# Performance work log

Hardware: AMD Instinct MI355X
Metric: run time of the kernel (lower is better)

The kernel has to match this reference:

```python
import jax, jax.numpy as jnp
import numpy as np

N_EMB = 1024
HEAD_SIZE = 128

def setup_inputs() -> dict:
    key = jax.random.key(0)
    kx, kq, kk, kv = jax.random.split(key, 4)
    s = 1.0 / np.sqrt(N_EMB)
    return {
        "x": jax.random.normal(kx, (4, 4096, N_EMB), dtype=jnp.float32),
        "Wq": jax.random.normal(kq, (N_EMB, HEAD_SIZE), dtype=jnp.float32) * s,
        "Wk": jax.random.normal(kk, (N_EMB, HEAD_SIZE), dtype=jnp.float32) * s,
        "Wv": jax.random.normal(kv, (N_EMB, HEAD_SIZE), dtype=jnp.float32) * s,
    }

def reference(x, Wq, Wk, Wv) -> jnp.ndarray:
    B, T, C = x.shape
    q = jnp.einsum('btc,cd->btd', x, Wq)  # [B,T,H]
    k = jnp.einsum('btc,cd->btd', x, Wk)
    v = jnp.einsum('btc,cd->btd', x, Wv)
    # NOTE: original scales by sqrt(n_emb), not sqrt(head_size)
    wei = jnp.einsum('btd,bsd->bts', q, k) / jnp.sqrt(jnp.asarray(C, x.dtype))
    causal = jnp.tril(jnp.ones((T, T), dtype=bool))
    wei = jnp.where(causal, wei, -jnp.inf)
    wei = jax.nn.softmax(wei, axis=-1)
    return jnp.einsum('bts,bsd->btd', wei, v)
```

## Files before the change

kernel.cpp:

```cpp
#include <hip/hip_runtime.h>
#include <hip/hip_bf16.h>


#define TSEQ 4096
#define NBATCH 4
#define CEMB 1024
#define HS 128
#define NWORK 272

typedef float  f32x4  __attribute__((ext_vector_type(4)));
typedef float  f32x16 __attribute__((ext_vector_type(16)));
typedef __bf16 bf16x4 __attribute__((ext_vector_type(4)));
typedef __bf16 bf16x8 __attribute__((ext_vector_type(8)));
typedef int    i32x2  __attribute__((ext_vector_type(2)));
typedef int    i32x4  __attribute__((ext_vector_type(4)));

__device__ __forceinline__ __bf16 f2b(float f) { return (__bf16)f; }
__device__ __forceinline__ float fexp2(float f) { return __builtin_amdgcn_exp2f(f); }

__device__ __forceinline__ void gl_lds16(const void* g, void* l) {
  __builtin_amdgcn_global_load_lds(
      (__attribute__((address_space(1))) void*)(g),
      (__attribute__((address_space(3))) void*)(l), 16, 0, 0);
}

__global__ void wtrans_kernel(const float* __restrict__ Wq,
                              const float* __restrict__ Wk,
                              const float* __restrict__ Wv,
                              __bf16* __restrict__ Wt) {
  const float* W = (blockIdx.y == 0) ? Wq : (blockIdx.y == 1) ? Wk : Wv;
  int g  = blockIdx.x * 256 + threadIdx.x;
  int n  = g & 127;
  int k0 = (g >> 7) * 8;
  bf16x8 v;
#pragma unroll
  for (int i = 0; i < 8; ++i) v[i] = f2b(W[(size_t)(k0 + i) * HS + n]);
  *(bf16x8*)(Wt + (size_t)blockIdx.y * HS * CEMB + (size_t)n * CEMB + k0) = v;
}

__global__ __launch_bounds__(128)
void proj_kernel(const float* __restrict__ x, const __bf16* __restrict__ Wt,
                 __bf16* __restrict__ qb, __bf16* __restrict__ kb,
                 __bf16* __restrict__ vt) {
  __shared__ __align__(16) __bf16 As[64 * 72];
  __shared__ __align__(16) __bf16 Bs[128 * 72];

  const int tid  = threadIdx.x;
  const int lane = tid & 63;
  const int w    = tid >> 6;
  const int l31  = lane & 31;
  const int half = lane >> 5;

  const int bid   = blockIdx.x;
  const int xcd   = bid & 7;
  const int rest  = bid >> 3;
  const int mat   = rest % 3;
  const int mslab = rest / 3;
  const int m0    = (xcd + 8 * mslab) * 64;
  const __bf16* Wm = Wt + (size_t)mat * HS * CEMB;

  f32x16 acc[2][2];
#pragma unroll
  for (int a = 0; a < 2; ++a)
#pragma unroll
    for (int b = 0; b < 2; ++b)
#pragma unroll
      for (int r = 0; r < 16; ++r) acc[a][b][r] = 0.f;

  const int srow = tid >> 3;
  const int soff = tid & 7;

  f32x4  pa[4][2];
  bf16x8 pb[8];
#pragma unroll
  for (int i = 0; i < 4; ++i) {
    const float* p = x + (size_t)(m0 + srow + 16 * i) * CEMB + soff * 8;
    pa[i][0] = *(const f32x4*)p;
    pa[i][1] = *(const f32x4*)(p + 4);
  }
#pragma unroll
  for (int i = 0; i < 8; ++i)
    pb[i] = *(const bf16x8*)(Wm + (size_t)(srow + 16 * i) * CEMB + soff * 8);

  for (int ks = 0; ks < CEMB; ks += 64) {
    __syncthreads();
#pragma unroll
    for (int i = 0; i < 4; ++i) {
      bf16x8 h;
#pragma unroll
      for (int j = 0; j < 4; ++j) {
        h[j]     = f2b(pa[i][0][j]);
        h[4 + j] = f2b(pa[i][1][j]);
      }
      *(bf16x8*)(As + (srow + 16 * i) * 72 + soff * 8) = h;
    }
#pragma unroll
    for (int i = 0; i < 8; ++i)
      *(bf16x8*)(Bs + (srow + 16 * i) * 72 + soff * 8) = pb[i];
    __syncthreads();
    if (ks + 64 < CEMB) {
#pragma unroll
      for (int i = 0; i < 4; ++i) {
        const float* p = x + (size_t)(m0 + srow + 16 * i) * CEMB + ks + 64 + soff * 8;
        pa[i][0] = *(const f32x4*)p;
        pa[i][1] = *(const f32x4*)(p + 4);
      }
#pragma unroll
      for (int i = 0; i < 8; ++i)
        pb[i] = *(const bf16x8*)(Wm + (size_t)(srow + 16 * i) * CEMB + ks + 64 + soff * 8);
    }
#pragma unroll
    for (int kc = 0; kc < 4; ++kc) {
      bf16x8 af[2], bf[2];
#pragma unroll
      for (int mi = 0; mi < 2; ++mi)
        af[mi] = *(const bf16x8*)(As + (mi * 32 + l31) * 72 + kc * 16 + half * 8);
#pragma unroll
      for (int ni = 0; ni < 2; ++ni)
        bf[ni] = *(const bf16x8*)(Bs + (64 * w + ni * 32 + l31) * 72 + kc * 16 + half * 8);
#pragma unroll
      for (int mi = 0; mi < 2; ++mi)
#pragma unroll
        for (int ni = 0; ni < 2; ++ni)
          acc[mi][ni] = __builtin_amdgcn_mfma_f32_32x32x16_bf16(
              af[mi], bf[ni], acc[mi][ni], 0, 0, 0);
    }
  }

  const float qscale = 1.4426950408889634f / 32.0f;
  if (mat == 0) {
#pragma unroll
    for (int mi = 0; mi < 2; ++mi)
#pragma unroll
      for (int ni = 0; ni < 2; ++ni) {
        int n = 64 * w + ni * 32 + l31;
#pragma unroll
        for (int r = 0; r < 16; ++r) {
          int m = m0 + mi * 32 + (r & 3) + 8 * (r >> 2) + 4 * half;
          qb[(size_t)m * HS + n] = f2b(acc[mi][ni][r] * qscale);
        }
      }
  } else if (mat == 1) {
#pragma unroll
    for (int mi = 0; mi < 2; ++mi)
#pragma unroll
      for (int ni = 0; ni < 2; ++ni) {
        int n = 64 * w + ni * 32 + l31;
#pragma unroll
        for (int r = 0; r < 16; ++r) {
          int m = m0 + mi * 32 + (r & 3) + 8 * (r >> 2) + 4 * half;
          kb[(size_t)m * HS + n] = f2b(acc[mi][ni][r]);
        }
      }
  } else {
    const int bt = m0 >> 12;
#pragma unroll
    for (int mi = 0; mi < 2; ++mi)
#pragma unroll
      for (int ni = 0; ni < 2; ++ni) {
        int n = 64 * w + ni * 32 + l31;
#pragma unroll
        for (int g = 0; g < 4; ++g) {
          bf16x4 pk;
#pragma unroll
          for (int d = 0; d < 4; ++d) pk[d] = f2b(acc[mi][ni][4 * g + d]);
          int tl = ((m0 + mi * 32) & 4095) + 8 * g + 4 * half;
          *(bf16x4*)(vt + ((size_t)bt * HS + n) * TSEQ + tl) = pk;
        }
      }
  }
}

__global__ __launch_bounds__(256)
void attn_kernel(const __bf16* __restrict__ qb, const __bf16* __restrict__ kb,
                 const __bf16* __restrict__ vt,
                 __bf16* __restrict__ Opart, float* __restrict__ Lpart) {
  __shared__ __align__(16) __bf16 Kt[64 * 128];
  __shared__ __align__(16) __bf16 Vtl[128 * 64];

  const int tid   = threadIdx.x;
  const int lane  = tid & 63;
  const int w     = tid >> 6;
  const int l31   = lane & 31;
  const int half  = lane >> 5;
  const int batch = blockIdx.y;
  const int xw    = blockIdx.x;

  int q = 0;
  while (q < 31 && xw >= (((q + 2) * (q + 2)) >> 2)) ++q;
  const int split = xw - (((q + 1) * (q + 1)) >> 2);
  const int ntile = 2 * (q + 1);
  const int nsp   = (q + 2) >> 1;
  const int tps   = (ntile + nsp - 1) / nsp;
  const int it0   = split * tps;
  const int it1   = min(it0 + tps, ntile);

  const int strip0 = q * 128 + w * 32;
  const size_t bbase = (size_t)batch * TSEQ;

  bf16x8 qf[8];
  {
    const __bf16* qr = qb + (bbase + strip0 + l31) * HS + half * 8;
#pragma unroll
    for (int kc = 0; kc < 8; ++kc) qf[kc] = *(const bf16x8*)(qr + kc * 16);
  }

  f32x16 o[4];
#pragma unroll
  for (int nt = 0; nt < 4; ++nt)
#pragma unroll
    for (int r = 0; r < 16; ++r) o[nt][r] = 0.f;
  float lsum = 0.f;

  for (int it = it0; it < it1; ++it) {
    const int c0 = it * 64;
    __syncthreads();
#pragma unroll
    for (int i = 0; i < 4; ++i) {
      int ck = i * 4 + w;
      {
        int r  = 4 * ck + (lane >> 4);
        int u1 = lane & 15;
        int u  = (u1 & 8) | ((u1 & 7) ^ (r & 7));
        gl_lds16(kb + (bbase + c0 + r) * HS + u * 8, &Kt[ck * 512]);
      }
      {
        int d  = 8 * ck + (lane >> 3);
        int u1 = lane & 7;
        int u  = u1 ^ (d & 7);
        gl_lds16(vt + ((size_t)batch * HS + d) * TSEQ + c0 + u * 8, &Vtl[ck * 512]);
      }
    }
    __syncthreads();

    if (c0 <= strip0 + 31) {
      i32x2 pkt[2][4];
#pragma unroll
      for (int t = 0; t < 2; ++t)
#pragma unroll
        for (int j = 0; j < 4; ++j) pkt[t][j] = (i32x2){0, 0};

#pragma unroll
      for (int t = 0; t < 2; ++t) {
        if (c0 + t * 32 <= strip0 + 31) {
          f32x16 s;
#pragma unroll
          for (int r = 0; r < 16; ++r) s[r] = 0.f;
#pragma unroll
          for (int kc = 0; kc < 8; ++kc) {
            int u  = 2 * kc + half;
            int up = (u & 8) | ((u & 7) ^ (l31 & 7));
            bf16x8 kf = *(const bf16x8*)(&Kt[(t * 32 + l31) * 128 + up * 8]);
            s = __builtin_amdgcn_mfma_f32_32x32x16_bf16(kf, qf[kc], s, 0, 0, 0);
          }
          if (c0 + t * 32 + 31 > strip0) {
#pragma unroll
            for (int r = 0; r < 16; ++r) {
              int key = c0 + t * 32 + (r & 3) + 8 * (r >> 2) + 4 * half;
              if (key > strip0 + l31) s[r] = -INFINITY;
            }
          }
          float p[16], ps = 0.f;
#pragma unroll
          for (int r = 0; r < 16; ++r) { p[r] = fexp2(s[r]); ps += p[r]; }
          lsum += ps;
#pragma unroll
          for (int j = 0; j < 4; ++j) {
            bf16x4 t4;
#pragma unroll
            for (int d = 0; d < 4; ++d) t4[d] = f2b(p[4 * j + d]);
            pkt[t][j] = __builtin_bit_cast(i32x2, t4);
          }
        }
      }
#pragma unroll
      for (int kk = 0; kk < 4; ++kk) {
        int t = kk >> 1, lo = (kk & 1) * 2;
        i32x2 a = pkt[t][lo], b = pkt[t][lo + 1];
        i32x2 ra, rb;
        ra.x = __shfl_xor(a.x, 32); ra.y = __shfl_xor(a.y, 32);
        rb.x = __shfl_xor(b.x, 32); rb.y = __shfl_xor(b.y, 32);
        i32x4 af4;
        af4.x = half ? rb.x : a.x;
        af4.y = half ? rb.y : a.y;
        af4.z = half ? b.x  : ra.x;
        af4.w = half ? b.y  : ra.y;
        bf16x8 af = __builtin_bit_cast(bf16x8, af4);
#pragma unroll
        for (int nt = 0; nt < 4; ++nt) {
          int up = (2 * kk + half) ^ (l31 & 7);
          bf16x8 vf = *(const bf16x8*)(&Vtl[(nt * 32 + l31) * 64 + up * 8]);
          o[nt] = __builtin_amdgcn_mfma_f32_32x32x16_bf16(af, vf, o[nt], 0, 0, 0);
        }
      }
    }
  }

  const size_t widx = (size_t)batch * NWORK + xw;
  __bf16* Op = Opart + widx * (128 * 128);
#pragma unroll
  for (int r = 0; r < 16; ++r) {
    int rloc = w * 32 + 4 * half + (r & 3) + 8 * (r >> 2);
#pragma unroll
    for (int nt = 0; nt < 4; ++nt)
      Op[rloc * 128 + nt * 32 + l31] = f2b(o[nt][r]);
  }
  lsum += __shfl_xor(lsum, 32);
  if (half == 0) Lpart[widx * 128 + w * 32 + l31] = lsum;
}

__global__ __launch_bounds__(256)
void reduce_kernel(const __bf16* __restrict__ Opart, const float* __restrict__ Lpart,
                   float* __restrict__ out) {
  const int batch = blockIdx.y;
  const int rowg  = blockIdx.x * 8 + (threadIdx.x >> 5);
  const int q = rowg >> 7;
  const int nsp = (q + 2) >> 1;
  const int off = ((q + 1) * (q + 1)) >> 2;
  const size_t wbase = (size_t)batch * NWORK + off;
  const int row128 = rowg & 127;
  const int c0 = (threadIdx.x & 31) * 4;

  float l = 0.f;
  for (int s = 0; s < nsp; ++s) l += Lpart[(wbase + s) * 128 + row128];
  const float inv = 1.0f / l;

  const __bf16* op = Opart + wbase * (128 * 128) + row128 * 128 + c0;
  f32x4 a = {0.f, 0.f, 0.f, 0.f};
  for (int s = 0; s < nsp; ++s) {
    bf16x4 v = *(const bf16x4*)(op + (size_t)s * 128 * 128);
#pragma unroll
    for (int j = 0; j < 4; ++j) a[j] += (float)v[j];
  }
  a *= inv;
  *(f32x4*)(out + ((size_t)batch * TSEQ + rowg) * HS + c0) = a;
}

extern "C" void kernel_launch(void* const* d_in, const int* in_sizes, int n_in,
                              void* d_out, int out_size, void* d_ws, size_t ws_size,
                              hipStream_t stream) {
  const float* x  = (const float*)d_in[0];
  const float* Wq = (const float*)d_in[1];
  const float* Wk = (const float*)d_in[2];
  const float* Wv = (const float*)d_in[3];
  float* out = (float*)d_out;

  char* ws = (char*)d_ws;
  __bf16* Wt = (__bf16*)ws;
  __bf16* qb = (__bf16*)(ws + 786432);
  __bf16* kb = (__bf16*)(ws + 786432 + 4194304);
  __bf16* vt = (__bf16*)(ws + 786432 + 2 * 4194304);
  __bf16* Opart = (__bf16*)(ws + 786432 + 3 * 4194304);
  float*  Lpart = (float*)(ws + 786432 + 3 * 4194304 +
                           (size_t)NBATCH * NWORK * 128 * 128 * 2);

  wtrans_kernel<<<dim3(64, 3), 256, 0, stream>>>(Wq, Wk, Wv, Wt);
  proj_kernel<<<dim3(768), 128, 0, stream>>>(x, Wt, qb, kb, vt);
  attn_kernel<<<dim3(NWORK, NBATCH), 256, 0, stream>>>(qb, kb, vt, Opart, Lpart);
  reduce_kernel<<<dim3(512, NBATCH), 256, 0, stream>>>(Opart, Lpart, out);
}
```

Before: 167.9 us.

## Double-buffer K/V tiles in LDS to overlap global loads with compute

The attention kernel now keeps two LDS buffers for the K and V tiles. It issues the direct-to-LDS loads for the next tile before computing on the current one, and replaces the two __syncthreads per iteration with raw s_barrier plus an explicit vmcnt wait. The goal is to hide global load latency behind the MFMA work. In exchange LDS use doubles to 64KB per block, which may lower occupancy, and the correctness of the hand-written vmcnt(8) depends on the compiler not emitting other vector memory ops in between.

```diff
diff --git a/kernel.cpp b/kernel.cpp
--- a/kernel.cpp
+++ b/kernel.cpp
@@ -175,8 +175,8 @@
 void attn_kernel(const __bf16* __restrict__ qb, const __bf16* __restrict__ kb,
                  const __bf16* __restrict__ vt,
                  __bf16* __restrict__ Opart, float* __restrict__ Lpart) {
-  __shared__ __align__(16) __bf16 Kt[64 * 128];
-  __shared__ __align__(16) __bf16 Vtl[128 * 64];
+  __shared__ __align__(16) __bf16 Kt[2][64 * 128];
+  __shared__ __align__(16) __bf16 Vtl[2][128 * 64];
 
   const int tid   = threadIdx.x;
   const int lane  = tid & 63;
@@ -194,6 +194,7 @@
   const int tps   = (ntile + nsp - 1) / nsp;
   const int it0   = split * tps;
   const int it1   = min(it0 + tps, ntile);
+  const int cnt   = it1 - it0;
 
   const int strip0 = q * 128 + w * 32;
   const size_t bbase = (size_t)batch * TSEQ;
@@ -212,9 +213,8 @@
     for (int r = 0; r < 16; ++r) o[nt][r] = 0.f;
   float lsum = 0.f;
 
-  for (int it = it0; it < it1; ++it) {
+  auto dma_tile = [&](int it, int b) {
     const int c0 = it * 64;
-    __syncthreads();
 #pragma unroll
     for (int i = 0; i < 4; ++i) {
       int ck = i * 4 + w;
@@ -222,17 +222,31 @@
         int r  = 4 * ck + (lane >> 4);
         int u1 = lane & 15;
         int u  = (u1 & 8) | ((u1 & 7) ^ (r & 7));
-        gl_lds16(kb + (bbase + c0 + r) * HS + u * 8, &Kt[ck * 512]);
+        gl_lds16(kb + (bbase + c0 + r) * HS + u * 8, &Kt[b][ck * 512]);
       }
       {
         int d  = 8 * ck + (lane >> 3);
         int u1 = lane & 7;
         int u  = u1 ^ (d & 7);
-        gl_lds16(vt + ((size_t)batch * HS + d) * TSEQ + c0 + u * 8, &Vtl[ck * 512]);
-      }
-    }
-    __syncthreads();
-
+        gl_lds16(vt + ((size_t)batch * HS + d) * TSEQ + c0 + u * 8, &Vtl[b][ck * 512]);
+      }
+    }
+  };
+
+  dma_tile(it0, 0);
+
+  for (int ii = 0; ii < cnt; ++ii) {
+    asm volatile("s_barrier" ::: "memory");
+    if (ii + 1 < cnt) {
+      dma_tile(it0 + ii + 1, (ii + 1) & 1);
+      asm volatile("s_waitcnt vmcnt(8)" ::: "memory");
+    } else {
+      asm volatile("s_waitcnt vmcnt(0)" ::: "memory");
+    }
+    asm volatile("s_barrier" ::: "memory");
+
+    const int c0 = (it0 + ii) * 64;
+    const int b  = ii & 1;
     if (c0 <= strip0 + 31) {
       i32x2 pkt[2][4];
 #pragma unroll
@@ -250,7 +264,7 @@
           for (int kc = 0; kc < 8; ++kc) {
             int u  = 2 * kc + half;
             int up = (u & 8) | ((u & 7) ^ (l31 & 7));
-            bf16x8 kf = *(const bf16x8*)(&Kt[(t * 32 + l31) * 128 + up * 8]);
+            bf16x8 kf = *(const bf16x8*)(&Kt[b][(t * 32 + l31) * 128 + up * 8]);
             s = __builtin_amdgcn_mfma_f32_32x32x16_bf16(kf, qf[kc], s, 0, 0, 0);
           }
           if (c0 + t * 32 + 31 > strip0) {
@@ -276,20 +290,20 @@
 #pragma unroll
       for (int kk = 0; kk < 4; ++kk) {
         int t = kk >> 1, lo = (kk & 1) * 2;
-        i32x2 a = pkt[t][lo], b = pkt[t][lo + 1];
+        i32x2 a = pkt[t][lo], bb2 = pkt[t][lo + 1];
         i32x2 ra, rb;
-        ra.x = __shfl_xor(a.x, 32); ra.y = __shfl_xor(a.y, 32);
-        rb.x = __shfl_xor(b.x, 32); rb.y = __shfl_xor(b.y, 32);
+        ra.x = __shfl_xor(a.x, 32);   ra.y = __shfl_xor(a.y, 32);
+        rb.x = __shfl_xor(bb2.x, 32); rb.y = __shfl_xor(bb2.y, 32);
         i32x4 af4;
-        af4.x = half ? rb.x : a.x;
-        af4.y = half ? rb.y : a.y;
-        af4.z = half ? b.x  : ra.x;
-        af4.w = half ? b.y  : ra.y;
+        af4.x = half ? rb.x  : a.x;
+        af4.y = half ? rb.y  : a.y;
+        af4.z = half ? bb2.x : ra.x;
+        af4.w = half ? bb2.y : ra.y;
         bf16x8 af = __builtin_bit_cast(bf16x8, af4);
 #pragma unroll
         for (int nt = 0; nt < 4; ++nt) {
           int up = (2 * kk + half) ^ (l31 & 7);
-          bf16x8 vf = *(const bf16x8*)(&Vtl[(nt * 32 + l31) * 64 + up * 8]);
+          bf16x8 vf = *(const bf16x8*)(&Vtl[b][(nt * 32 + l31) * 64 + up * 8]);
           o[nt] = __builtin_amdgcn_mfma_f32_32x32x16_bf16(af, vf, o[nt], 0, 0, 0);
         }
       }
```

Result: no change. 170.1 us (+1.3%).

## Pre-swizzle weights into MFMA fragment layout and load B operand directly to registers

Applied to the files above, without the earlier changes.

The weight transpose kernel now writes W in a per-lane MFMA fragment order, so each wave in the projection kernel can load its B operands straight from global memory into registers with coalesced 16-byte loads. This removes the B tile from LDS, along with its stores and reads. The cost is more registers for double-buffered B fragments, and each wave loads only its own half of the weights instead of sharing them. It also frees LDS, which may allow higher occupancy.

```diff
diff --git a/kernel.cpp b/kernel.cpp
--- a/kernel.cpp
+++ b/kernel.cpp
@@ -27,23 +27,27 @@
 __global__ void wtrans_kernel(const float* __restrict__ Wq,
                               const float* __restrict__ Wk,
                               const float* __restrict__ Wv,
-                              __bf16* __restrict__ Wt) {
-  const float* W = (blockIdx.y == 0) ? Wq : (blockIdx.y == 1) ? Wk : Wv;
-  int g  = blockIdx.x * 256 + threadIdx.x;
-  int n  = g & 127;
-  int k0 = (g >> 7) * 8;
+                              __bf16* __restrict__ Wtf) {
+  const int mat = blockIdx.y;
+  const float* W = (mat == 0) ? Wq : (mat == 1) ? Wk : Wv;
+  int g    = blockIdx.x * 256 + threadIdx.x;
+  int lane = g & 63;
+  int kcg  = (g >> 6) & 63;
+  int nt   = g >> 12;
+  int n    = nt * 32 + (lane & 31);
+  int k0   = kcg * 16 + (lane >> 5) * 8;
   bf16x8 v;
 #pragma unroll
-  for (int i = 0; i < 8; ++i) v[i] = f2b(W[(size_t)(k0 + i) * HS + n]);
-  *(bf16x8*)(Wt + (size_t)blockIdx.y * HS * CEMB + (size_t)n * CEMB + k0) = v;
+  for (int j = 0; j < 8; ++j) v[j] = f2b(W[(size_t)(k0 + j) * HS + n]);
+  size_t idx = ((size_t)(mat * 4 + nt) * 64 + kcg) * 64 + lane;
+  *(bf16x8*)(Wtf + idx * 8) = v;
 }
 
 __global__ __launch_bounds__(128)
-void proj_kernel(const float* __restrict__ x, const __bf16* __restrict__ Wt,
+void proj_kernel(const float* __restrict__ x, const __bf16* __restrict__ Wtf,
                  __bf16* __restrict__ qb, __bf16* __restrict__ kb,
                  __bf16* __restrict__ vt) {
   __shared__ __align__(16) __bf16 As[64 * 72];
-  __shared__ __align__(16) __bf16 Bs[128 * 72];
 
   const int tid  = threadIdx.x;
   const int lane = tid & 63;
@@ -57,7 +61,6 @@
   const int mat   = rest % 3;
   const int mslab = rest / 3;
   const int m0    = (xcd + 8 * mslab) * 64;
-  const __bf16* Wm = Wt + (size_t)mat * HS * CEMB;
 
   f32x16 acc[2][2];
 #pragma unroll
@@ -70,17 +73,21 @@
   const int srow = tid >> 3;
   const int soff = tid & 7;
 
-  f32x4  pa[4][2];
-  bf16x8 pb[8];
+  f32x4 pa[4][2];
 #pragma unroll
   for (int i = 0; i < 4; ++i) {
     const float* p = x + (size_t)(m0 + srow + 16 * i) * CEMB + soff * 8;
     pa[i][0] = *(const f32x4*)p;
     pa[i][1] = *(const f32x4*)(p + 4);
   }
-#pragma unroll
-  for (int i = 0; i < 8; ++i)
-    pb[i] = *(const bf16x8*)(Wm + (size_t)(srow + 16 * i) * CEMB + soff * 8);
+  bf16x8 pB[2][4], pBn[2][4];
+#pragma unroll
+  for (int ni = 0; ni < 2; ++ni) {
+    size_t base = ((size_t)(mat * 4 + 2 * w + ni) * 64) * 64 + lane;
+#pragma unroll
+    for (int kc = 0; kc < 4; ++kc)
+      pB[ni][kc] = *(const bf16x8*)(Wtf + (base + (size_t)kc * 64) * 8);
+  }
 
   for (int ks = 0; ks < CEMB; ks += 64) {
     __syncthreads();
@@ -94,11 +101,9 @@
       }
       *(bf16x8*)(As + (srow + 16 * i) * 72 + soff * 8) = h;
     }
-#pragma unroll
-    for (int i = 0; i < 8; ++i)
-      *(bf16x8*)(Bs + (srow + 16 * i) * 72 + soff * 8) = pb[i];
     __syncthreads();
     if (ks + 64 < CEMB) {
+      const int kbn = (ks >> 4) + 4;
 #pragma unroll
       for (int i = 0; i < 4; ++i) {
         const float* p = x + (size_t)(m0 + srow + 16 * i) * CEMB + ks + 64 + soff * 8;
@@ -106,25 +111,30 @@
         pa[i][1] = *(const f32x4*)(p + 4);
       }
 #pragma unroll
-      for (int i = 0; i < 8; ++i)
-        pb[i] = *(const bf16x8*)(Wm + (size_t)(srow + 16 * i) * CEMB + ks + 64 + soff * 8);
+      for (int ni = 0; ni < 2; ++ni) {
+        size_t base = ((size_t)(mat * 4 + 2 * w + ni) * 64 + kbn) * 64 + lane;
+#pragma unroll
+        for (int kc = 0; kc < 4; ++kc)
+          pBn[ni][kc] = *(const bf16x8*)(Wtf + (base + (size_t)kc * 64) * 8);
+      }
     }
 #pragma unroll
     for (int kc = 0; kc < 4; ++kc) {
-      bf16x8 af[2], bf[2];
+      bf16x8 af[2];
 #pragma unroll
       for (int mi = 0; mi < 2; ++mi)
         af[mi] = *(const bf16x8*)(As + (mi * 32 + l31) * 72 + kc * 16 + half * 8);
 #pragma unroll
-      for (int ni = 0; ni < 2; ++ni)
-        bf[ni] = *(const bf16x8*)(Bs + (64 * w + ni * 32 + l31) * 72 + kc * 16 + half * 8);
-#pragma unroll
       for (int mi = 0; mi < 2; ++mi)
 #pragma unroll
         for (int ni = 0; ni < 2; ++ni)
           acc[mi][ni] = __builtin_amdgcn_mfma_f32_32x32x16_bf16(
-              af[mi], bf[ni], acc[mi][ni], 0, 0, 0);
-    }
+              af[mi], pB[ni][kc], acc[mi][ni], 0, 0, 0);
+    }
+#pragma unroll
+    for (int ni = 0; ni < 2; ++ni)
+#pragma unroll
+      for (int kc = 0; kc < 4; ++kc) pB[ni][kc] = pBn[ni][kc];
   }
 
   const float qscale = 1.4426950408889634f / 32.0f;
@@ -346,7 +356,7 @@
   float* out = (float*)d_out;
 
   char* ws = (char*)d_ws;
-  __bf16* Wt = (__bf16*)ws;
+  __bf16* Wtf = (__bf16*)ws;
   __bf16* qb = (__bf16*)(ws + 786432);
   __bf16* kb = (__bf16*)(ws + 786432 + 4194304);
   __bf16* vt = (__bf16*)(ws + 786432 + 2 * 4194304);
@@ -354,8 +364,8 @@
   float*  Lpart = (float*)(ws + 786432 + 3 * 4194304 +
                            (size_t)NBATCH * NWORK * 128 * 128 * 2);
 
-  wtrans_kernel<<<dim3(64, 3), 256, 0, stream>>>(Wq, Wk, Wv, Wt);
-  proj_kernel<<<dim3(768), 128, 0, stream>>>(x, Wt, qb, kb, vt);
+  wtrans_kernel<<<dim3(64, 3), 256, 0, stream>>>(Wq, Wk, Wv, Wtf);
+  proj_kernel<<<dim3(768), 128, 0, stream>>>(x, Wtf, qb, kb, vt);
   attn_kernel<<<dim3(NWORK, NBATCH), 256, 0, stream>>>(qb, kb, vt, Opart, Lpart);
   reduce_kernel<<<dim3(512, NBATCH), 256, 0, stream>>>(Opart, Lpart, out);
 }
```

Result: no change. 168.0 us (+0.1%).
